# Performance work log

Measured on AMD Instinct MI355X. Metric: run time of the kernel, lower is better.

The kernel has to match this reference:

```python
import jax, jax.numpy as jnp
import numpy as np

N_EMB = 1024
N_HEAD = 16
EPS = 1e-5


def _linear_params(key, fan_in, fan_out):
    k1, k2 = jax.random.split(key)
    lim = 1.0 / np.sqrt(fan_in)
    W = jax.random.uniform(k1, (fan_in, fan_out), minval=-lim, maxval=lim, dtype=jnp.float32)
    b = jax.random.uniform(k2, (fan_out,), minval=-lim, maxval=lim, dtype=jnp.float32)
    return W, b


def setup_inputs() -> dict:
    key = jax.random.key(0)
    ks = jax.random.split(key, 8)
    x = jax.random.normal(ks[0], (4, 2048, N_EMB), dtype=jnp.float32)
    Wk, bk = _linear_params(ks[1], N_EMB, N_EMB)
    Wq, bq = _linear_params(ks[2], N_EMB, N_EMB)
    Wv, bv = _linear_params(ks[3], N_EMB, N_EMB)
    Wp, bp = _linear_params(ks[4], N_EMB, N_EMB)
    W1, b1 = _linear_params(ks[5], N_EMB, 4 * N_EMB)
    W2, b2 = _linear_params(ks[6], 4 * N_EMB, N_EMB)
    return {
        "x": x,
        "ln1_g": jnp.ones((N_EMB,), jnp.float32), "ln1_b": jnp.zeros((N_EMB,), jnp.float32),
        "Wk": Wk, "bk": bk, "Wq": Wq, "bq": bq, "Wv": Wv, "bv": bv, "Wp": Wp, "bp": bp,
        "ln2_g": jnp.ones((N_EMB,), jnp.float32), "ln2_b": jnp.zeros((N_EMB,), jnp.float32),
        "W1": W1, "b1": b1, "W2": W2, "b2": b2,
        "cond_len": 256,
    }


def _layernorm(x, g, b):
    mu = jnp.mean(x, axis=-1, keepdims=True)
    var = jnp.mean(jnp.square(x - mu), axis=-1, keepdims=True)
    return (x - mu) * jax.lax.rsqrt(var + EPS) * g + b


def _hybrid_mask(T, cond_len):
    # rows attend to all conditioning columns; causal within the remaining block
    i = jnp.arange(T)[:, None]
    j = jnp.arange(T)[None, :]
    return (j < cond_len) | ((i >= cond_len) & (j >= cond_len) & (j <= i))  # [T,T] bool


def _block(x, ln1_g, ln1_b, Wk, bk, Wq, bq, Wv, bv, Wp, bp, ln2_g, ln2_b, W1, b1, W2, b2, cond_len):
    B, T, C = x.shape
    hd = C // N_HEAD
    h = _layernorm(x, ln1_g, ln1_b)
    # QKV: [B,T,C] -> [B,H,T,hd]
    q = (h @ Wq + bq).reshape(B, T, N_HEAD, hd).transpose(0, 2, 1, 3)
    k = (h @ Wk + bk).reshape(B, T, N_HEAD, hd).transpose(0, 2, 1, 3)
    v = (h @ Wv + bv).reshape(B, T, N_HEAD, hd).transpose(0, 2, 1, 3)
    att = jnp.einsum('bhqd,bhkd->bhqk', q, k) * (1.0 / np.sqrt(hd))
    mask = _hybrid_mask(T, cond_len)
    att = jnp.where(mask, att, -jnp.inf)
    att = jax.nn.softmax(att, axis=-1)
    y = jnp.einsum('bhqk,bhkd->bhqd', att, v)
    y = y.transpose(0, 2, 1, 3).reshape(B, T, C)
    x = x + (y @ Wp + bp)
    h2 = _layernorm(x, ln2_g, ln2_b)
    m = jax.nn.gelu(h2 @ W1 + b1, approximate=False) @ W2 + b2
    return x + m


def reference(x, ln1_g, ln1_b, Wk, bk, Wq, bq, Wv, bv, Wp, bp, ln2_g, ln2_b, W1, b1, W2, b2, cond_len):
    return _block(x, ln1_g, ln1_b, Wk, bk, Wq, bq, Wv, bv, Wp, bp, ln2_g, ln2_b, W1, b1, W2, b2, cond_len)
```

## Files before the change

### kernel.cpp

```cpp
#include <hip/hip_runtime.h>

typedef __bf16 bf16;
typedef __attribute__((ext_vector_type(4))) __bf16 bf16x4;
typedef __attribute__((ext_vector_type(8))) __bf16 bf16x8;
typedef __attribute__((ext_vector_type(4))) float f32x4;

__device__ __forceinline__ void stage16(const bf16* g, bf16* l) {
  __builtin_amdgcn_global_load_lds(
      (const __attribute__((address_space(1))) void*)g,
      (__attribute__((address_space(3))) void*)l, 16, 0, 0);
}

__global__ __launch_bounds__(256)
void transpose_f32_bf16(const float* __restrict__ src, bf16* __restrict__ dst, int R, int C)
{
  __shared__ bf16 tile[32][33];
  const int tx = threadIdx.x & 31, ty = threadIdx.x >> 5;
  const int c0 = blockIdx.x * 32, r0 = blockIdx.y * 32;
#pragma unroll
  for (int i = 0; i < 4; ++i)
    tile[ty + i * 8][tx] = (bf16)src[(size_t)(r0 + ty + i * 8) * C + c0 + tx];
  __syncthreads();
#pragma unroll
  for (int i = 0; i < 4; ++i)
    dst[(size_t)(c0 + ty + i * 8) * R + r0 + tx] = tile[tx][ty + i * 8];
}

__global__ __launch_bounds__(256)
void ln_f32_bf16(const float* __restrict__ x, const float* __restrict__ g,
                 const float* __restrict__ bta, bf16* __restrict__ out)
{
  const int row = blockIdx.x * 4 + (threadIdx.x >> 6);
  const int l = threadIdx.x & 63;
  const float* xr = x + (size_t)row * 1024 + l * 16;
  f32x4 a[4];
#pragma unroll
  for (int i = 0; i < 4; ++i) a[i] = ((const f32x4*)xr)[i];
  float s = 0.f, s2 = 0.f;
#pragma unroll
  for (int i = 0; i < 4; ++i)
#pragma unroll
    for (int jj = 0; jj < 4; ++jj) { float vv = a[i][jj]; s += vv; s2 += vv * vv; }
#pragma unroll
  for (int m = 1; m < 64; m <<= 1) { s += __shfl_xor(s, m); s2 += __shfl_xor(s2, m); }
  const float mu = s * (1.0f / 1024.0f);
  const float var = s2 * (1.0f / 1024.0f) - mu * mu;
  const float rs = rsqrtf(var + 1e-5f);
  f32x4 gv[4], bv[4];
#pragma unroll
  for (int i = 0; i < 4; ++i) {
    gv[i] = ((const f32x4*)(g + l * 16))[i];
    bv[i] = ((const f32x4*)(bta + l * 16))[i];
  }
  bf16x8 o0, o1;
#pragma unroll
  for (int i = 0; i < 8; ++i) {
    float v0 = a[i >> 2][i & 3];
    float v1 = a[2 + (i >> 2)][i & 3];
    o0[i] = (bf16)((v0 - mu) * rs * gv[i >> 2][i & 3] + bv[i >> 2][i & 3]);
    o1[i] = (bf16)((v1 - mu) * rs * gv[2 + (i >> 2)][i & 3] + bv[2 + (i >> 2)][i & 3]);
  }
  bf16* orow = out + (size_t)row * 1024 + l * 16;
  ((bf16x8*)orow)[0] = o0;
  ((bf16x8*)orow)[1] = o1;
}

template <int EPI>
__global__ __launch_bounds__(256)
void gemm_bt(const bf16* __restrict__ A, const bf16* __restrict__ Bt,
             const float* __restrict__ bias, const float* __restrict__ biasK,
             const float* __restrict__ biasV,
             void* __restrict__ out, void* __restrict__ outK, void* __restrict__ outV,
             const float* __restrict__ res, int M, int N, int K)
{
  __shared__ bf16 As[2][128 * 32];
  __shared__ bf16 Bs[2][128 * 32];
  const int tid = threadIdx.x;
  const int l = tid & 63;
  const int w = tid >> 6;
  const int wm = w >> 1, wn = w & 1;
  const int m0 = blockIdx.x * 128;
  const int n0 = blockIdx.y * 128;

  const int srow = tid >> 2;
  const int sG8 = ((tid & 3) ^ ((tid >> 3) & 3)) * 8;
  const bf16* gA = A + (size_t)(m0 + srow) * K + sG8;
  const bf16* gB = Bt + (size_t)(n0 + srow) * K + sG8;
  const int ldsOff = srow * 32 + (tid & 3) * 8;

  const int lrow = l & 15;
  const int rdsl = ((l >> 4) ^ ((lrow >> 1) & 3)) * 8;

  f32x4 acc[4][4] = {};
  const int KT = K >> 5;

#define STAGE(buf, k0)                                            \
  do {                                                            \
    stage16(gA + (k0), &As[buf][ldsOff]);                         \
    stage16(gA + (size_t)64 * K + (k0), &As[buf][2048 + ldsOff]); \
    stage16(gB + (k0), &Bs[buf][ldsOff]);                         \
    stage16(gB + (size_t)64 * K + (k0), &Bs[buf][2048 + ldsOff]); \
  } while (0)

  STAGE(0, 0);

  for (int kt = 0; kt < KT; ++kt) {
    const int cur = kt & 1;
    __builtin_amdgcn_s_barrier();
    if (kt + 1 < KT) {
      STAGE(cur ^ 1, (kt + 1) << 5);
      asm volatile("s_waitcnt vmcnt(4)" ::: "memory");
    } else {
      asm volatile("s_waitcnt vmcnt(0)" ::: "memory");
    }
    __builtin_amdgcn_sched_barrier(0);
    __builtin_amdgcn_s_barrier();

    bf16x8 af[4], bfv[4];
#pragma unroll
    for (int i = 0; i < 4; ++i)
      af[i] = *(const bf16x8*)&As[cur][(wm * 64 + i * 16 + lrow) * 32 + rdsl];
#pragma unroll
    for (int i = 0; i < 4; ++i)
      bfv[i] = *(const bf16x8*)&Bs[cur][(wn * 64 + i * 16 + lrow) * 32 + rdsl];
#pragma unroll
    for (int mi = 0; mi < 4; ++mi)
#pragma unroll
      for (int ni = 0; ni < 4; ++ni)
        acc[mi][ni] = __builtin_amdgcn_mfma_f32_16x16x32_bf16(af[mi], bfv[ni], acc[mi][ni], 0, 0, 0);
  }
#undef STAGE

  const int seg = n0 >> 10;
  const float* bp = (EPI == 0) ? (seg == 0 ? bias : (seg == 1 ? biasK : biasV)) : bias;
#pragma unroll
  for (int mi = 0; mi < 4; ++mi) {
#pragma unroll
    for (int ni = 0; ni < 4; ++ni) {
      const int colg = n0 + wn * 64 + ni * 16 + lrow;
      const int col = (EPI == 0) ? (colg & 1023) : colg;
      const float bv = bp[col];
#pragma unroll
      for (int j = 0; j < 4; ++j) {
        const int row = m0 + wm * 64 + mi * 16 + (l >> 4) * 4 + j;
        float val = acc[mi][ni][j] + bv;
        if constexpr (EPI == 0) {
          const int b = row >> 11, t = row & 2047, hh = col >> 6, d = col & 63;
          if (seg == 0)
            ((bf16*)out)[(((size_t)(b * 16 + hh) * 2048 + t) * 64) + d] = (bf16)(val * 0.125f);
          else if (seg == 1)
            ((bf16*)outK)[(((size_t)(b * 16 + hh) * 2048 + t) * 64) + d] = (bf16)val;
          else
            ((bf16*)outV)[(((size_t)(b * 16 + hh) * 64 + d) * 2048) + t] = (bf16)val;
        } else if constexpr (EPI == 3) {
          ((float*)out)[(size_t)row * 1024 + col] = val + res[(size_t)row * 1024 + col];
        } else if constexpr (EPI == 4) {
          const float ge = 0.5f * val * (1.0f + erff(val * 0.70710678118f));
          ((bf16*)out)[(size_t)row * N + col] = (bf16)ge;
        } else if constexpr (EPI == 5) {
          ((float*)out)[(size_t)row * 1024 + col] = val + res[(size_t)row * 1024 + col];
        }
      }
    }
  }
}

__global__ __launch_bounds__(512)
void attn_kernel(const bf16* __restrict__ q, const bf16* __restrict__ k,
                 const bf16* __restrict__ v, bf16* __restrict__ y,
                 const int* __restrict__ condp)
{
  __shared__ bf16 Ks[2][64 * 72];
  __shared__ bf16 Vs[2][64 * 72];
  __shared__ char PsB[8][2048];
  const int tid = threadIdx.x, l = tid & 63, w = tid >> 6;
  const int bx = blockIdx.x;
  const int qt = 15 - (bx >> 6);
  const int bh = bx & 63;
  const int bb = bh >> 4, hh = bh & 15;
  const int cond = condp[0];
  const int iLo = qt * 128;
  const size_t base = (size_t)bh * 2048 * 64;

  const int lrow = l & 15;
  const int g = l >> 4;
  const int lslot = g * 8;

  const int qrow = iLo + w * 16 + lrow;
  const bf16x8 bq0 = *(const bf16x8*)(q + base + (size_t)qrow * 64 + lslot);
  const bf16x8 bq1 = *(const bf16x8*)(q + base + (size_t)qrow * 64 + 32 + lslot);

  f32x4 o[4] = {};
  float m = -1e30f, lsum = 0.f;

  const int ckt = (cond + 63) >> 6;
  int nkt = ((iLo + 127) >> 6) + 1;
  if (nkt < ckt) nkt = ckt;
  const int wHi = iLo + w * 16 + 15;

  const int kr = tid >> 3;
  const int ks8 = (tid & 7) * 8;
  const bf16* kp = k + base + (size_t)kr * 64 + ks8;
  const bf16* vp = v + base + (size_t)kr * 2048 + ks8;

  bf16x8 rk = *(const bf16x8*)kp;
  bf16x8 rv = *(const bf16x8*)vp;
  *(bf16x8*)&Ks[0][kr * 72 + ks8] = rk;
  *(bf16x8*)&Vs[0][kr * 72 + ks8] = rv;
  __syncthreads();

  char* psw = PsB[w];

  for (int kt = 0; kt < nkt; ++kt) {
    const int cur = kt & 1;
    const int j0 = kt << 6;
    const bool pf = (kt + 1 < nkt);
    if (pf) {
      rk = *(const bf16x8*)(kp + (size_t)(j0 + 64) * 64);
      rv = *(const bf16x8*)(vp + j0 + 64);
    }

    const bool active = (j0 < cond) || (j0 <= wHi);
    if (active) {
      f32x4 sfr[4];
      __builtin_amdgcn_s_setprio(1);
#pragma unroll
      for (int nf = 0; nf < 4; ++nf) {
        f32x4 s = {};
        bf16x8 ka0 = *(const bf16x8*)&Ks[cur][(nf * 16 + lrow) * 72 + lslot];
        bf16x8 ka1 = *(const bf16x8*)&Ks[cur][(nf * 16 + lrow) * 72 + 32 + lslot];
        s = __builtin_amdgcn_mfma_f32_16x16x32_bf16(ka0, bq0, s, 0, 0, 0);
        s = __builtin_amdgcn_mfma_f32_16x16x32_bf16(ka1, bq1, s, 0, 0, 0);
        sfr[nf] = s;
      }
      __builtin_amdgcn_s_setprio(0);

      const bool safe = (j0 + 63 < cond) || (j0 + 63 <= iLo + w * 16);
      if (!safe) {
#pragma unroll
        for (int nf = 0; nf < 4; ++nf)
#pragma unroll
          for (int j = 0; j < 4; ++j) {
            const int kc = j0 + nf * 16 + g * 4 + j;
            const bool ok = (kc < cond) || (kc <= qrow);
            sfr[nf][j] = ok ? sfr[nf][j] : -1e30f;
          }
      }

      float pmax = sfr[0][0];
#pragma unroll
      for (int nf = 0; nf < 4; ++nf)
#pragma unroll
        for (int j = 0; j < 4; ++j) pmax = fmaxf(pmax, sfr[nf][j]);
      pmax = fmaxf(pmax, __shfl_xor(pmax, 16));
      pmax = fmaxf(pmax, __shfl_xor(pmax, 32));

      const bool resc = !__all(pmax - m <= 8.0f);
      if (resc) {
        const float mnew = fmaxf(m, pmax);
        const float alpha = __expf(m - mnew);
        m = mnew;
        lsum *= alpha;
        float ar[4];
#pragma unroll
        for (int j = 0; j < 4; ++j) ar[j] = __shfl(alpha, (l & 48) | (g * 4 + j));
#pragma unroll
        for (int df = 0; df < 4; ++df)
#pragma unroll
          for (int j = 0; j < 4; ++j) o[df][j] *= ar[j];
      }

      float rsum = 0.f;
#pragma unroll
      for (int nf = 0; nf < 4; ++nf) {
        bf16x4 pk;
#pragma unroll
        for (int j = 0; j < 4; ++j) {
          const float p = __expf(sfr[nf][j] - m);
          rsum += p;
          pk[j] = (bf16)p;
        }
        const int slot = 2 * nf + (g >> 1);
        const int boff = lrow * 128 + ((slot ^ (lrow & 7)) << 4) + (g & 1) * 8;
        *(bf16x4*)(psw + boff) = pk;
      }
      rsum += __shfl_xor(rsum, 16);
      rsum += __shfl_xor(rsum, 32);
      lsum += rsum;

      const int r0b = lrow * 128 + (((g) ^ (lrow & 7)) << 4);
      const int r1b = lrow * 128 + (((g + 4) ^ (lrow & 7)) << 4);
      const bf16x8 pa0 = *(const bf16x8*)(psw + r0b);
      const bf16x8 pa1 = *(const bf16x8*)(psw + r1b);
      __builtin_amdgcn_s_setprio(1);
#pragma unroll
      for (int df = 0; df < 4; ++df) {
        bf16x8 v0 = *(const bf16x8*)&Vs[cur][(df * 16 + lrow) * 72 + lslot];
        bf16x8 v1 = *(const bf16x8*)&Vs[cur][(df * 16 + lrow) * 72 + 32 + lslot];
        o[df] = __builtin_amdgcn_mfma_f32_16x16x32_bf16(pa0, v0, o[df], 0, 0, 0);
        o[df] = __builtin_amdgcn_mfma_f32_16x16x32_bf16(pa1, v1, o[df], 0, 0, 0);
      }
      __builtin_amdgcn_s_setprio(0);
    }

    if (pf) {
      *(bf16x8*)&Ks[cur ^ 1][kr * 72 + ks8] = rk;
      *(bf16x8*)&Vs[cur ^ 1][kr * 72 + ks8] = rv;
    }
    __syncthreads();
  }

  float lr[4];
#pragma unroll
  for (int j = 0; j < 4; ++j) lr[j] = 1.0f / __shfl(lsum, (l & 48) | (g * 4 + j));
#pragma unroll
  for (int df = 0; df < 4; ++df)
#pragma unroll
    for (int j = 0; j < 4; ++j) {
      const int irow = iLo + w * 16 + g * 4 + j;
      y[((size_t)bb * 2048 + irow) * 1024 + hh * 64 + df * 16 + lrow] = (bf16)(o[df][j] * lr[j]);
    }
}

extern "C" void kernel_launch(void* const* d_in, const int* in_sizes, int n_in,
                              void* d_out, int out_size, void* d_ws, size_t ws_size,
                              hipStream_t stream) {
  const float* x    = (const float*)d_in[0];
  const float* ln1g = (const float*)d_in[1];
  const float* ln1b = (const float*)d_in[2];
  const float* Wk   = (const float*)d_in[3];
  const float* bk   = (const float*)d_in[4];
  const float* Wq   = (const float*)d_in[5];
  const float* bq   = (const float*)d_in[6];
  const float* Wv   = (const float*)d_in[7];
  const float* bv   = (const float*)d_in[8];
  const float* Wp   = (const float*)d_in[9];
  const float* bpb  = (const float*)d_in[10];
  const float* ln2g = (const float*)d_in[11];
  const float* ln2b = (const float*)d_in[12];
  const float* W1   = (const float*)d_in[13];
  const float* b1   = (const float*)d_in[14];
  const float* W2   = (const float*)d_in[15];
  const float* b2   = (const float*)d_in[16];
  const int*  cond  = (const int*)d_in[17];
  float* out = (float*)d_out;

  char* ws = (char*)d_ws;
  const size_t MB = 1024ull * 1024ull;
  if (ws_size < 136 * MB) return;

  bf16*  WqkvT = (bf16*)(ws + 0 * MB);
  bf16*  WpT   = (bf16*)(ws + 6 * MB);
  bf16*  W1T   = (bf16*)(ws + 8 * MB);
  bf16*  W2T   = (bf16*)(ws + 16 * MB);
  float* x2    = (float*)(ws + 24 * MB);
  bf16*  hbuf  = (bf16*)(ws + 56 * MB);
  bf16*  qb    = (bf16*)(ws + 72 * MB);
  bf16*  kb    = (bf16*)(ws + 88 * MB);
  bf16*  vb    = (bf16*)(ws + 104 * MB);
  bf16*  yb    = (bf16*)(ws + 120 * MB);
  bf16*  m1    = (bf16*)(ws + 72 * MB);

  dim3 blk(256);
  transpose_f32_bf16<<<dim3(32, 32), blk, 0, stream>>>(Wq, WqkvT,                1024, 1024);
  transpose_f32_bf16<<<dim3(32, 32), blk, 0, stream>>>(Wk, WqkvT + 1024 * 1024,  1024, 1024);
  transpose_f32_bf16<<<dim3(32, 32), blk, 0, stream>>>(Wv, WqkvT + 2048 * 1024,  1024, 1024);
  transpose_f32_bf16<<<dim3(32, 32), blk, 0, stream>>>(Wp, WpT, 1024, 1024);
  transpose_f32_bf16<<<dim3(128, 32), blk, 0, stream>>>(W1, W1T, 1024, 4096);
  transpose_f32_bf16<<<dim3(32, 128), blk, 0, stream>>>(W2, W2T, 4096, 1024);

  ln_f32_bf16<<<2048, blk, 0, stream>>>(x, ln1g, ln1b, hbuf);

  gemm_bt<0><<<dim3(64, 24), blk, 0, stream>>>(hbuf, WqkvT, bq, bk, bv,
                                               qb, kb, vb, nullptr, 8192, 3072, 1024);

  attn_kernel<<<dim3(1024), dim3(512), 0, stream>>>(qb, kb, vb, yb, cond);

  gemm_bt<3><<<dim3(64, 8), blk, 0, stream>>>(yb, WpT, bpb, nullptr, nullptr,
                                              x2, nullptr, nullptr, x, 8192, 1024, 1024);
  ln_f32_bf16<<<2048, blk, 0, stream>>>(x2, ln2g, ln2b, hbuf);
  gemm_bt<4><<<dim3(64, 32), blk, 0, stream>>>(hbuf, W1T, b1, nullptr, nullptr,
                                               m1, nullptr, nullptr, nullptr, 8192, 4096, 1024);
  gemm_bt<5><<<dim3(64, 8), blk, 0, stream>>>(m1, W2T, b2, nullptr, nullptr,
                                              out, nullptr, nullptr, x2, 8192, 1024, 4096);
}
```

Baseline: 413.8 us.

## Enlarge GEMM tiles to 256x256 with 8 waves and interleaved staged prefetch

Rewrites the bf16 GEMM to use 256x256 output tiles, 512 threads and a K-step of 64. Each wave now owns a 128x64 sub-tile. Global-to-LDS prefetch of the next K-block is split into four pieces interleaved between MFMA phases, with s_setprio raising priority during the MFMA bursts. The aim is more data reuse per LDS byte and better overlap of loads with matrix math. In exchange the grids shrink: the projection and W2 GEMMs drop to 128 blocks and QKV to 384 blocks, which can leave compute units idle or create tail waves. LDS use per block also grows to 128KB.

```diff
diff --git a/kernel.cpp b/kernel.cpp
--- a/kernel.cpp
+++ b/kernel.cpp
@@ -66,75 +66,133 @@
 }
 
 template <int EPI>
-__global__ __launch_bounds__(256)
+__global__ __launch_bounds__(512, 2)
 void gemm_bt(const bf16* __restrict__ A, const bf16* __restrict__ Bt,
              const float* __restrict__ bias, const float* __restrict__ biasK,
              const float* __restrict__ biasV,
              void* __restrict__ out, void* __restrict__ outK, void* __restrict__ outV,
              const float* __restrict__ res, int M, int N, int K)
 {
-  __shared__ bf16 As[2][128 * 32];
-  __shared__ bf16 Bs[2][128 * 32];
+  __shared__ bf16 As[2][2][128][64];
+  __shared__ bf16 Bs[2][2][128][64];
   const int tid = threadIdx.x;
   const int l = tid & 63;
   const int w = tid >> 6;
-  const int wm = w >> 1, wn = w & 1;
-  const int m0 = blockIdx.x * 128;
-  const int n0 = blockIdx.y * 128;
-
-  const int srow = tid >> 2;
-  const int sG8 = ((tid & 3) ^ ((tid >> 3) & 3)) * 8;
-  const bf16* gA = A + (size_t)(m0 + srow) * K + sG8;
-  const bf16* gB = Bt + (size_t)(n0 + srow) * K + sG8;
-  const int ldsOff = srow * 32 + (tid & 3) * 8;
+  const int wm = w >> 2;
+  const int wn = w & 3;
+  const int m0 = blockIdx.x * 256;
+  const int n0 = blockIdx.y * 256;
+
+  const int srow = tid >> 3;
+  const int sslot = tid & 7;
+  const int gcolsw = ((sslot ^ (srow & 7)) << 3);
+  const bf16* gA = A + (size_t)(m0 + srow) * K + gcolsw;
+  const bf16* gB = Bt + (size_t)(n0 + srow) * K + gcolsw;
 
   const int lrow = l & 15;
-  const int rdsl = ((l >> 4) ^ ((lrow >> 1) & 3)) * 8;
-
-  f32x4 acc[4][4] = {};
-  const int KT = K >> 5;
-
-#define STAGE(buf, k0)                                            \
-  do {                                                            \
-    stage16(gA + (k0), &As[buf][ldsOff]);                         \
-    stage16(gA + (size_t)64 * K + (k0), &As[buf][2048 + ldsOff]); \
-    stage16(gB + (k0), &Bs[buf][ldsOff]);                         \
-    stage16(gB + (size_t)64 * K + (k0), &Bs[buf][2048 + ldsOff]); \
+  const int lgrp = l >> 4;
+
+  f32x4 acc[8][4] = {};
+  const int KT = K >> 6;
+
+#define STA(buf, h, kb)                                                          \
+  do {                                                                           \
+    stage16(gA + (size_t)(h) * 128 * K + (kb), &As[buf][h][srow][sslot * 8]);    \
+    stage16(gA + (size_t)((h) * 128 + 64) * K + (kb), &As[buf][h][64 + srow][sslot * 8]); \
   } while (0)
-
-  STAGE(0, 0);
+#define STB(buf, h, kb)                                                          \
+  do {                                                                           \
+    stage16(gB + (size_t)(h) * 128 * K + (kb), &Bs[buf][h][srow][sslot * 8]);    \
+    stage16(gB + (size_t)((h) * 128 + 64) * K + (kb), &Bs[buf][h][64 + srow][sslot * 8]); \
+  } while (0)
+#define RDA(dst, mi, ks)                                                         \
+  do {                                                                           \
+    const int row_ = (mi) * 16 + lrow;                                           \
+    const int sl_ = ((((ks) * 4 + lgrp) ^ (row_ & 7)) << 3);                     \
+    dst = *(const bf16x8*)&As[cur][wm][row_][sl_];                               \
+  } while (0)
+#define RDB(dst, ni, ks)                                                         \
+  do {                                                                           \
+    const int row_ = (wn & 1) * 64 + (ni) * 16 + lrow;                           \
+    const int sl_ = ((((ks) * 4 + lgrp) ^ (row_ & 7)) << 3);                     \
+    dst = *(const bf16x8*)&Bs[cur][wn >> 1][row_][sl_];                          \
+  } while (0)
+
+  STA(0, 0, 0); STA(0, 1, 0); STB(0, 0, 0); STB(0, 1, 0);
 
   for (int kt = 0; kt < KT; ++kt) {
     const int cur = kt & 1;
-    __builtin_amdgcn_s_barrier();
-    if (kt + 1 < KT) {
-      STAGE(cur ^ 1, (kt + 1) << 5);
-      asm volatile("s_waitcnt vmcnt(4)" ::: "memory");
-    } else {
-      asm volatile("s_waitcnt vmcnt(0)" ::: "memory");
-    }
+    const int nxt = cur ^ 1;
+    const int kb = (kt + 1) << 6;
+    const bool pf = (kt + 1 < KT);
+
+    __builtin_amdgcn_s_barrier();
+    if (pf) STA(nxt, 0, kb);
+    if (pf) asm volatile("s_waitcnt vmcnt(2)" ::: "memory");
+    else    asm volatile("s_waitcnt vmcnt(0)" ::: "memory");
     __builtin_amdgcn_sched_barrier(0);
     __builtin_amdgcn_s_barrier();
 
-    bf16x8 af[4], bfv[4];
-#pragma unroll
-    for (int i = 0; i < 4; ++i)
-      af[i] = *(const bf16x8*)&As[cur][(wm * 64 + i * 16 + lrow) * 32 + rdsl];
-#pragma unroll
-    for (int i = 0; i < 4; ++i)
-      bfv[i] = *(const bf16x8*)&Bs[cur][(wn * 64 + i * 16 + lrow) * 32 + rdsl];
+    bf16x8 a[4][2], b[4][2];
+#pragma unroll
+    for (int mi = 0; mi < 4; ++mi) { RDA(a[mi][0], mi, 0); RDA(a[mi][1], mi, 1); }
+#pragma unroll
+    for (int ni = 0; ni < 4; ++ni) { RDB(b[ni][0], ni, 0); RDB(b[ni][1], ni, 1); }
+    __builtin_amdgcn_s_setprio(1);
 #pragma unroll
     for (int mi = 0; mi < 4; ++mi)
 #pragma unroll
-      for (int ni = 0; ni < 4; ++ni)
-        acc[mi][ni] = __builtin_amdgcn_mfma_f32_16x16x32_bf16(af[mi], bfv[ni], acc[mi][ni], 0, 0, 0);
+      for (int ni = 0; ni < 2; ++ni)
+#pragma unroll
+        for (int ks = 0; ks < 2; ++ks)
+          acc[mi][ni] = __builtin_amdgcn_mfma_f32_16x16x32_bf16(a[mi][ks], b[ni][ks], acc[mi][ni], 0, 0, 0);
+    __builtin_amdgcn_s_setprio(0);
+    __builtin_amdgcn_s_barrier();
+    if (pf) STA(nxt, 1, kb);
+    __builtin_amdgcn_s_setprio(1);
+#pragma unroll
+    for (int mi = 0; mi < 4; ++mi)
+#pragma unroll
+      for (int ni = 2; ni < 4; ++ni)
+#pragma unroll
+        for (int ks = 0; ks < 2; ++ks)
+          acc[mi][ni] = __builtin_amdgcn_mfma_f32_16x16x32_bf16(a[mi][ks], b[ni][ks], acc[mi][ni], 0, 0, 0);
+    __builtin_amdgcn_s_setprio(0);
+    __builtin_amdgcn_s_barrier();
+#pragma unroll
+    for (int mi = 0; mi < 4; ++mi) { RDA(a[mi][0], 4 + mi, 0); RDA(a[mi][1], 4 + mi, 1); }
+    if (pf) STB(nxt, 0, kb);
+    __builtin_amdgcn_s_setprio(1);
+#pragma unroll
+    for (int mi = 0; mi < 4; ++mi)
+#pragma unroll
+      for (int ni = 0; ni < 2; ++ni)
+#pragma unroll
+        for (int ks = 0; ks < 2; ++ks)
+          acc[4 + mi][ni] = __builtin_amdgcn_mfma_f32_16x16x32_bf16(a[mi][ks], b[ni][ks], acc[4 + mi][ni], 0, 0, 0);
+    __builtin_amdgcn_s_setprio(0);
+    __builtin_amdgcn_s_barrier();
+    if (pf) STB(nxt, 1, kb);
+    __builtin_amdgcn_s_setprio(1);
+#pragma unroll
+    for (int mi = 0; mi < 4; ++mi)
+#pragma unroll
+      for (int ni = 2; ni < 4; ++ni)
+#pragma unroll
+        for (int ks = 0; ks < 2; ++ks)
+          acc[4 + mi][ni] = __builtin_amdgcn_mfma_f32_16x16x32_bf16(a[mi][ks], b[ni][ks], acc[4 + mi][ni], 0, 0, 0);
+    __builtin_amdgcn_s_setprio(0);
+    __builtin_amdgcn_s_barrier();
   }
-#undef STAGE
+#undef STA
+#undef STB
+#undef RDA
+#undef RDB
 
   const int seg = n0 >> 10;
   const float* bp = (EPI == 0) ? (seg == 0 ? bias : (seg == 1 ? biasK : biasV)) : bias;
 #pragma unroll
-  for (int mi = 0; mi < 4; ++mi) {
+  for (int mi = 0; mi < 8; ++mi) {
 #pragma unroll
     for (int ni = 0; ni < 4; ++ni) {
       const int colg = n0 + wn * 64 + ni * 16 + lrow;
@@ -142,7 +200,7 @@
       const float bv = bp[col];
 #pragma unroll
       for (int j = 0; j < 4; ++j) {
-        const int row = m0 + wm * 64 + mi * 16 + (l >> 4) * 4 + j;
+        const int row = m0 + wm * 128 + mi * 16 + (l >> 4) * 4 + j;
         float val = acc[mi][ni][j] + bv;
         if constexpr (EPI == 0) {
           const int b = row >> 11, t = row & 2047, hh = col >> 6, d = col & 63;
@@ -371,16 +429,16 @@
 
   ln_f32_bf16<<<2048, blk, 0, stream>>>(x, ln1g, ln1b, hbuf);
 
-  gemm_bt<0><<<dim3(64, 24), blk, 0, stream>>>(hbuf, WqkvT, bq, bk, bv,
-                                               qb, kb, vb, nullptr, 8192, 3072, 1024);
+  gemm_bt<0><<<dim3(32, 12), dim3(512), 0, stream>>>(hbuf, WqkvT, bq, bk, bv,
+                                                     qb, kb, vb, nullptr, 8192, 3072, 1024);
 
   attn_kernel<<<dim3(1024), dim3(512), 0, stream>>>(qb, kb, vb, yb, cond);
 
-  gemm_bt<3><<<dim3(64, 8), blk, 0, stream>>>(yb, WpT, bpb, nullptr, nullptr,
-                                              x2, nullptr, nullptr, x, 8192, 1024, 1024);
+  gemm_bt<3><<<dim3(32, 4), dim3(512), 0, stream>>>(yb, WpT, bpb, nullptr, nullptr,
+                                                    x2, nullptr, nullptr, x, 8192, 1024, 1024);
   ln_f32_bf16<<<2048, blk, 0, stream>>>(x2, ln2g, ln2b, hbuf);
-  gemm_bt<4><<<dim3(64, 32), blk, 0, stream>>>(hbuf, W1T, b1, nullptr, nullptr,
-                                               m1, nullptr, nullptr, nullptr, 8192, 4096, 1024);
-  gemm_bt<5><<<dim3(64, 8), blk, 0, stream>>>(m1, W2T, b2, nullptr, nullptr,
-                                              out, nullptr, nullptr, x2, 8192, 1024, 4096);
-}
+  gemm_bt<4><<<dim3(32, 16), dim3(512), 0, stream>>>(hbuf, W1T, b1, nullptr, nullptr,
+                                                     m1, nullptr, nullptr, nullptr, 8192, 4096, 1024);
+  gemm_bt<5><<<dim3(32, 4), dim3(512), 0, stream>>>(m1, W2T, b2, nullptr, nullptr,
+                                                    out, nullptr, nullptr, x2, 8192, 1024, 4096);
+}
```

Measured after the change: 471.6 us. 14.0% more time.
